# Kernel tuning notes

Hardware: AMD Instinct MI355X
Metric: run time of the kernel (lower is better)

## Reference

```python
import jax, jax.numpy as jnp
import numpy as np

N, E, B, H, L = 50000, 500000, 64, 64, 4


def setup_inputs() -> dict:
    key = jax.random.key(0)
    ks = jax.random.split(key, 32)
    def w(k, shp, fan_in):
        s = 1.0 / np.sqrt(fan_in)
        return jax.random.uniform(k, shp, jnp.float32, -s, s)
    inp = {
        "v0": jax.random.normal(ks[0], (N, 1), jnp.float32),
        "v1": jax.random.normal(ks[1], (N, 1), jnp.float32),
        "dist": jax.random.uniform(ks[2], (E, 1), jnp.float32),
        "edge_index": jax.random.randint(ks[3], (2, E), 0, N, jnp.int32),
        "batch": jnp.sort(jax.random.randint(ks[4], (N,), 0, B, jnp.int32)),
        "batch_size": B,
        # embeddings / per-input linears
        "wte": jax.random.normal(ks[5], (2, H), jnp.float32),
        "W_in0": w(ks[6], (H, 1), 1), "b_in0": w(ks[7], (H,), 1),
        "W_in1": w(ks[8], (H, 1), 1), "b_in1": w(ks[9], (H,), 1),
        "W_out0": w(ks[10], (1, H), H), "b_out0": w(ks[11], (1,), H),
        "W_out1": w(ks[12], (1, H), H), "b_out1": w(ks[13], (1,), H),
        "W_edge": w(ks[14], (H, 1), 1), "b_edge": w(ks[15], (H,), 1),
        # shared GraphBlock (ModuleList([block]*L) shares weights)
        "W_el": w(ks[16], (H, 2 * H), 2 * H), "b_el": w(ks[17], (H,), 2 * H),
        "W_n1": w(ks[18], (4 * H, 3 * H), 3 * H), "b_n1": w(ks[19], (4 * H,), 3 * H),
        "W_n2": w(ks[20], (H, 4 * H), 4 * H), "b_n2": w(ks[21], (H,), 4 * H),
        "W_gl": w(ks[22], (H, 2 * H), 2 * H), "b_gl": w(ks[23], (H,), 2 * H),
        # shared LSTMCell
        "W_ih": w(ks[24], (4 * H, H), H), "W_hh": w(ks[25], (4 * H, H), H),
        "b_ih": w(ks[26], (4 * H,), H), "b_hh": w(ks[27], (4 * H,), H),
    }
    return inp


def _forward(v0, v1, dist, edge_index, batch, batch_size,
             wte, W_in0, b_in0, W_in1, b_in1, W_out0, b_out0, W_out1, b_out1,
             W_edge, b_edge, W_el, b_el, W_n1, b_n1, W_n2, b_n2, W_gl, b_gl,
             W_ih, W_hh, b_ih, b_hh):
    # x = sum_i (type_embedding_i + Linear_i(v_i))  -> [N, H]
    x = (wte[0] + v0 @ W_in0.T + b_in0) + (wte[1] + v1 @ W_in1.T + b_in1)
    e = dist @ W_edge.T + b_edge                      # [E, H]
    u = jnp.zeros((batch_size, x.shape[-1]), x.dtype)  # [B, H]
    row, col = edge_index[0], edge_index[1]
    n_nodes = x.shape[0]
    cs = []
    for _ in range(L):  # shared weights across layers (faithful to [block]*L)
        # edge MLP on gathered source features, scatter-max to destination nodes
        msg = jax.nn.relu(jnp.concatenate([x[row], e], axis=-1) @ W_el.T + b_el)
        agg = jax.ops.segment_max(msg, col, num_segments=n_nodes)
        agg = jnp.where(jnp.isfinite(agg), agg, 0.0)  # empty segments -> 0
        # node MLP with residual
        h1 = jax.nn.relu(jnp.concatenate([agg, x, u[batch]], axis=-1) @ W_n1.T + b_n1)
        x = x + h1 @ W_n2.T + b_n2
        # global update: per-graph max over nodes
        x_u = jax.ops.segment_max(x, batch, num_segments=batch_size)
        x_u = jnp.where(jnp.isfinite(x_u), x_u, 0.0)
        u = u + jax.nn.relu(jnp.concatenate([x_u, u], axis=-1) @ W_gl.T + b_gl)
        # LSTMCell with zero initial (h, c) every layer (hidden_states=None path)
        gates = u @ W_ih.T + b_ih + b_hh  # h_prev = 0 so W_hh term vanishes
        i_g, f_g, g_g, o_g = jnp.split(gates, 4, axis=-1)
        c = jax.nn.sigmoid(i_g) * jnp.tanh(g_g)        # c_prev = 0
        u = jax.nn.sigmoid(o_g) * jnp.tanh(c)
        cs.append(c)
    outs = jnp.stack([x @ W_out0.T + b_out0, x @ W_out1.T + b_out1])  # [2, N, 1]
    return outs, jnp.stack(cs)  # ([2,N,1], [L,B,H])


def reference(v0, v1, dist, edge_index, batch, batch_size,
              wte, W_in0, b_in0, W_in1, b_in1, W_out0, b_out0, W_out1, b_out1,
              W_edge, b_edge, W_el, b_el, W_n1, b_n1, W_n2, b_n2, W_gl, b_gl,
              W_ih, W_hh, b_ih, b_hh):
    return _forward(v0, v1, dist, edge_index, batch, batch_size,
                    wte, W_in0, b_in0, W_in1, b_in1, W_out0, b_out0, W_out1, b_out1,
                    W_edge, b_edge, W_el, b_el, W_n1, b_n1, W_n2, b_n2, W_gl, b_gl,
                    W_ih, W_hh, b_ih, b_hh)
```

## Files before the change

kernel.cpp:

```cpp
#include <hip/hip_runtime.h>


typedef __attribute__((ext_vector_type(8))) short short8;
typedef __attribute__((ext_vector_type(4))) float f32x4;

__device__ __forceinline__ unsigned short f2bf(float f) {
  union { float f; unsigned u; } v; v.f = f;
  unsigned r = v.u + 0x7FFFu + ((v.u >> 16) & 1u);
  return (unsigned short)(r >> 16);
}
__device__ __forceinline__ float bf2f(unsigned short s) {
  return __uint_as_float((unsigned)s << 16);
}
__device__ __forceinline__ unsigned enc_ordered(float f) {
  unsigned u = __float_as_uint(f);
  return (u >> 31) ? ~u : (u | 0x80000000u);
}

__global__ void k_init(const float* __restrict__ v0, const float* __restrict__ v1,
                       const float* __restrict__ wte,
                       const float* __restrict__ Wi0, const float* __restrict__ bi0,
                       const float* __restrict__ Wi1, const float* __restrict__ bi1,
                       const int* __restrict__ batch,
                       int* __restrict__ gstart, int* __restrict__ gend,
                       float* __restrict__ x,
                       float* __restrict__ u, unsigned* __restrict__ xu_enc,
                       unsigned short* __restrict__ W1b, unsigned short* __restrict__ W2b,
                       unsigned short* __restrict__ Welb,
                       const float* __restrict__ W_n1, const float* __restrict__ W_n2,
                       const float* __restrict__ W_el,
                       const float* __restrict__ b_el,
                       const float* __restrict__ W_edge, const float* __restrict__ b_edge,
                       float* __restrict__ p, float* __restrict__ q,
                       float* __restrict__ c0, float* __restrict__ c1,
                       float* __restrict__ c2,
                       int* __restrict__ deg, int* __restrict__ cur, int N) {
  int gt = blockIdx.x * 256 + threadIdx.x;
  int NH = N * 64;
  if (gt < NH) {
    int n = gt >> 6, h = gt & 63;
    x[gt] = wte[h] + wte[64 + h] + bi0[h] + bi1[h] + v0[n] * Wi0[h] + v1[n] * Wi1[h];
    if (h == 0) {
      int bg = batch[n];
      if (n == 0 || batch[n - 1] != bg) gstart[bg] = n;
      if (n == N - 1 || batch[n + 1] != bg) gend[bg] = n + 1;
    }
    return;
  }
  int i = gt - NH;
  if (i < 4096) {
    u[i] = 0.f;
  } else if (i < 8192) {
    xu_enc[i - 4096] = 0x007FFFFFu;
  } else if (i < 8192 + 49152) {
    int j = i - 8192;
    W1b[j] = f2bf(W_n1[j]);
  } else if (i < 8192 + 49152 + 16384) {
    int j = i - 57344;
    W2b[j] = f2bf(W_n2[j]);
  } else if (i < 77824) {
    int j = i - 73728;
    Welb[j] = f2bf(W_el[(j >> 6) * 128 + (j & 63)]);
  } else if (i < 77824 + N) {
    deg[i - 77824] = 0;
  } else if (i < 77824 + 2 * N) {
    cur[i - 77824 - N] = 0;
  } else if (i < 77824 + 2 * N + 64) {
    int h = i - 77824 - 2 * N;
    float pp = 0.f, qq = 0.f, s0 = 0.f, s1 = 0.f, s2 = 0.f;
    for (int k = 0; k < 64; ++k) {
      float w2 = W_el[h * 128 + 64 + k];
      pp += w2 * W_edge[k];
      qq += w2 * b_edge[k];
      float w1 = W_el[h * 128 + k];
      float base = wte[k] + wte[64 + k] + bi0[k] + bi1[k];
      s0 += w1 * base;
      s1 += w1 * Wi0[k];
      s2 += w1 * Wi1[k];
    }
    p[h] = pp; q[h] = qq + b_el[h];
    c0[h] = s0; c1[h] = s1; c2[h] = s2;
  }
}

__global__ __launch_bounds__(256) void k_hist(const int* __restrict__ eidx,
                                              int* __restrict__ deg, int E) {
  int e = blockIdx.x * 256 + threadIdx.x;
  if (e < E) atomicAdd(&deg[eidx[E + e]], 1);
}

__global__ __launch_bounds__(256) void k_scan1(const int* __restrict__ deg,
                                               int* __restrict__ off,
                                               int* __restrict__ bsum, int N) {
  __shared__ int s[256];
  int b = blockIdx.x, t = threadIdx.x;
  int i0 = b * 512 + t * 2;
  int v0 = (i0 < N) ? deg[i0] : 0;
  int v1 = (i0 + 1 < N) ? deg[i0 + 1] : 0;
  int sum = v0 + v1;
  s[t] = sum;
  __syncthreads();
  for (int d = 1; d < 256; d <<= 1) {
    int val = (t >= d) ? s[t - d] : 0;
    __syncthreads();
    s[t] += val;
    __syncthreads();
  }
  int excl = s[t] - sum;
  if (i0 < N) off[i0] = excl + v0;
  if (i0 + 1 < N) off[i0 + 1] = excl + v0 + v1;
  if (t == 255) bsum[b] = s[t];
}

__global__ void k_scan2(int* __restrict__ bsum, int nb) {
  __shared__ int s[128];
  int t = threadIdx.x;
  int v = (t < nb) ? bsum[t] : 0;
  s[t] = v;
  __syncthreads();
  for (int d = 1; d < 128; d <<= 1) {
    int val = (t >= d) ? s[t - d] : 0;
    __syncthreads();
    s[t] += val;
    __syncthreads();
  }
  if (t < nb) bsum[t] = s[t] - v;
}

__global__ __launch_bounds__(256) void k_scatter(const int* __restrict__ eidx,
                                                 const float* __restrict__ dist,
                                                 const int* __restrict__ off,
                                                 const int* __restrict__ bsum,
                                                 int* __restrict__ cur,
                                                 uint2* __restrict__ spack, int E) {
  int e = blockIdx.x * 256 + threadIdx.x;
  if (e >= E) return;
  int c = eidx[E + e];
  int base = (c == 0) ? 0 : (off[c - 1] + bsum[(c - 1) >> 9]);
  int pos = base + atomicAdd(&cur[c], 1);
  spack[pos] = make_uint2((unsigned)eidx[e] | ((unsigned)(c & 31) << 27),
                          __float_as_uint(dist[e]));
}

template <int MODE>
__global__ __launch_bounds__(256) void k_node(
    const int* __restrict__ off, const int* __restrict__ bsum,
    const uint2* __restrict__ spack,
    const float* __restrict__ p, const float* __restrict__ q,
    const float* __restrict__ c0, const float* __restrict__ c1,
    const float* __restrict__ c2,
    const float* __restrict__ v0, const float* __restrict__ v1,
    float* __restrict__ x, unsigned short* __restrict__ y_bf,
    const int* __restrict__ batch, const float* __restrict__ u,
    const unsigned short* __restrict__ W1b, const unsigned short* __restrict__ W2b,
    const unsigned short* __restrict__ Welb,
    const float* __restrict__ b_n1, const float* __restrict__ b_n2,
    unsigned* __restrict__ xu_enc,
    float* __restrict__ bmaxA, float* __restrict__ bmaxB,
    int* __restrict__ bgidA, int* __restrict__ bgidB,
    const float* __restrict__ Wo0, const float* __restrict__ bo0,
    const float* __restrict__ Wo1, const float* __restrict__ bo1,
    float* __restrict__ outp, int N) {
  __shared__ __align__(16) char inb[32 * 384];
  __shared__ __align__(16) char h1T[32 * 512];
  __shared__ uint2 smeta[256];
  __shared__ int sgb[32];
  int t = threadIdx.x;
  int n0 = blockIdx.x * 32;
  int lane = t & 63, wv = t >> 6;
  int lr = lane & 15;
  int lk8 = (lane >> 4) << 3;
  int jo = (lane >> 4) << 2;
  int swzr = (lr & 7) << 4;
  int h0 = wv * 16 + jo;

  float4 xo[2];
#pragma unroll
  for (int nt = 0; nt < 2; ++nt) {
    int node = n0 + nt * 16 + lr;
    xo[nt] = (node < N) ? *(const float4*)(x + (size_t)node * 64 + h0)
                        : make_float4(0.f, 0.f, 0.f, 0.f);
  }
  int nd_s = t >> 3, ko = t & 7;
  int node_s = n0 + nd_s;
  float4 ua = make_float4(0.f, 0.f, 0.f, 0.f), ub = ua;
  if (node_s < N) {
    int g = batch[node_s];
    const float4* u4 = (const float4*)u;
    ua = u4[g * 16 + ko * 2];
    ub = u4[g * 16 + ko * 2 + 1];
  }
  if (t < 32) sgb[t] = batch[min(n0 + t, N - 1)];

  int* aggi = (int*)h1T;
#pragma unroll
  for (int i = 0; i < 8; ++i) aggi[t + i * 256] = 0;

#pragma unroll
  for (int nt = 0; nt < 2; ++nt) {
    int nd = nt * 16 + lr;
    unsigned lo = (unsigned)f2bf(xo[nt].x) | ((unsigned)f2bf(xo[nt].y) << 16);
    unsigned hi = (unsigned)f2bf(xo[nt].z) | ((unsigned)f2bf(xo[nt].w) << 16);
    *(uint2*)(inb + nd * 384 + ((128 + h0 * 2) ^ ((nd & 7) << 4))) = make_uint2(lo, hi);
  }
  {
    int swz = (nd_s & 7) << 4;
    uint4 uv;
    uv.x = f2bf(ua.x) | ((unsigned)f2bf(ua.y) << 16);
    uv.y = f2bf(ua.z) | ((unsigned)f2bf(ua.w) << 16);
    uv.z = f2bf(ub.x) | ((unsigned)f2bf(ub.y) << 16);
    uv.w = f2bf(ub.z) | ((unsigned)f2bf(ub.w) << 16);
    *(uint4*)(inb + nd_s * 384 + ((256 + ko * 16) ^ swz)) = uv;
  }
  __syncthreads();

  {
    int last = min(n0 + 31, N - 1);
    int ebase = (n0 == 0) ? 0 : (off[n0 - 1] + bsum[(n0 - 1) >> 9]);
    int eend = off[last] + bsum[last >> 9];
    int total = eend - ebase;
    int q4 = total >> 2;
    int wb = ebase + wv * q4;
    int we = (wv == 3) ? eend : (wb + q4);
    uint2* sm = smeta + wv * 64;
    int half = lane >> 5, l31 = lane & 31;
    const unsigned* y32 = (const unsigned*)y_bf + l31;
    float2 p2 = *(const float2*)(p + 2 * l31);
    float2 q2 = *(const float2*)(q + 2 * l31);
    float2 c02 = make_float2(0.f, 0.f), c12 = c02, c22 = c02;
    if (MODE == 0) {
      c02 = *(const float2*)(c0 + 2 * l31);
      c12 = *(const float2*)(c1 + 2 * l31);
      c22 = *(const float2*)(c2 + 2 * l31);
    }
    float m0 = 0.f, m1 = 0.f;
    int ccur = -1;
    uint2 r = make_uint2(0u, 0u);
    if (wb < we) {
      int cnt = min(64, we - wb);
      if (lane < cnt) r = spack[wb + lane];
    }
    for (int cb = wb; cb < we; cb += 64) {
      int ccnt = min(64, we - cb);
      sm[lane] = r;
      int nb = cb + 64;
      if (nb < we) {
        int ncnt = we - nb;
        if (lane < ncnt) r = spack[nb + lane];
      }
      int nfull = ccnt >> 1;
      int i = 0;
      for (; i + 8 <= nfull; i += 8) {
        uint2 e[8]; unsigned yd[8]; float va[8], vb[8];
#pragma unroll
        for (int k = 0; k < 8; ++k) e[k] = sm[2 * (i + k) + half];
#pragma unroll
        for (int k = 0; k < 8; ++k) {
          unsigned row = e[k].x & 0x07FFFFFFu;
          if (MODE == 0) { va[k] = v0[row]; vb[k] = v1[row]; }
          else yd[k] = y32[row << 5];
        }
#pragma unroll
        for (int k = 0; k < 8; ++k) {
          float y0f, y1f;
          if (MODE == 0) {
            y0f = fmaf(vb[k], c22.x, fmaf(va[k], c12.x, c02.x));
            y1f = fmaf(vb[k], c22.y, fmaf(va[k], c12.y, c02.y));
          } else {
            y0f = __uint_as_float(yd[k] << 16);
            y1f = __uint_as_float(yd[k] & 0xFFFF0000u);
          }
          float d = __uint_as_float(e[k].y);
          float g0 = fmaxf(fmaf(d, p2.x, y0f + q2.x), 0.f);
          float g1 = fmaxf(fmaf(d, p2.y, y1f + q2.y), 0.f);
          int c = (int)(e[k].x >> 27);
          if (c != ccur) {
            if (ccur >= 0) {
              atomicMax(&aggi[ccur * 64 + 2 * l31], __float_as_int(m0));
              atomicMax(&aggi[ccur * 64 + 2 * l31 + 1], __float_as_int(m1));
            }
            ccur = c; m0 = g0; m1 = g1;
          } else { m0 = fmaxf(m0, g0); m1 = fmaxf(m1, g1); }
        }
      }
      for (; 2 * i < ccnt; ++i) {
        int idx = 2 * i + half;
        bool val = idx < ccnt;
        uint2 e = sm[val ? idx : 0];
        unsigned row = e.x & 0x07FFFFFFu;
        float y0f, y1f;
        if (MODE == 0) {
          float a = v0[row], b = v1[row];
          y0f = fmaf(b, c22.x, fmaf(a, c12.x, c02.x));
          y1f = fmaf(b, c22.y, fmaf(a, c12.y, c02.y));
        } else {
          unsigned yd = y32[row << 5];
          y0f = __uint_as_float(yd << 16);
          y1f = __uint_as_float(yd & 0xFFFF0000u);
        }
        float d = __uint_as_float(e.y);
        float g0 = val ? fmaxf(fmaf(d, p2.x, y0f + q2.x), 0.f) : 0.f;
        float g1 = val ? fmaxf(fmaf(d, p2.y, y1f + q2.y), 0.f) : 0.f;
        int c = val ? (int)(e.x >> 27) : ccur;
        if (c != ccur) {
          if (ccur >= 0) {
            atomicMax(&aggi[ccur * 64 + 2 * l31], __float_as_int(m0));
            atomicMax(&aggi[ccur * 64 + 2 * l31 + 1], __float_as_int(m1));
          }
          ccur = c; m0 = g0; m1 = g1;
        } else { m0 = fmaxf(m0, g0); m1 = fmaxf(m1, g1); }
      }
    }
    if (ccur >= 0) {
      atomicMax(&aggi[ccur * 64 + 2 * l31], __float_as_int(m0));
      atomicMax(&aggi[ccur * 64 + 2 * l31 + 1], __float_as_int(m1));
    }
  }
  __syncthreads();

  {
    int swz = (nd_s & 7) << 4;
    const float4* ag4 = (const float4*)(h1T);
    float4 aa = ag4[nd_s * 16 + ko * 2];
    float4 ab = ag4[nd_s * 16 + ko * 2 + 1];
    uint4 av;
    av.x = f2bf(aa.x) | ((unsigned)f2bf(aa.y) << 16);
    av.y = f2bf(aa.z) | ((unsigned)f2bf(aa.w) << 16);
    av.z = f2bf(ab.x) | ((unsigned)f2bf(ab.y) << 16);
    av.w = f2bf(ab.z) | ((unsigned)f2bf(ab.w) << 16);
    *(uint4*)(inb + nd_s * 384 + ((ko * 16) ^ swz)) = av;
  }
  __syncthreads();

  int w = wv;

  f32x4 acc[4][2];
#pragma unroll
  for (int ot = 0; ot < 4; ++ot)
#pragma unroll
    for (int nt = 0; nt < 2; ++nt) acc[ot][nt] = (f32x4){0.f, 0.f, 0.f, 0.f};
  const unsigned short* W1p = W1b + (w * 64 + lr) * 192 + lk8;
#pragma unroll
  for (int ks = 0; ks < 6; ++ks) {
    int kb = ks * 64 + lk8 * 2;
    short8 b0 = *(const short8*)(inb + lr * 384 + (kb ^ swzr));
    short8 b1 = *(const short8*)(inb + (16 + lr) * 384 + (kb ^ swzr));
#pragma unroll
    for (int ot = 0; ot < 4; ++ot) {
      short8 a = *(const short8*)(W1p + ot * (16 * 192) + ks * 32);
      acc[ot][0] = __builtin_amdgcn_mfma_f32_16x16x32_bf16(a, b0, acc[ot][0], 0, 0, 0);
      acc[ot][1] = __builtin_amdgcn_mfma_f32_16x16x32_bf16(a, b1, acc[ot][1], 0, 0, 0);
    }
  }
  __syncthreads();
#pragma unroll
  for (int ot = 0; ot < 4; ++ot) {
    int o = w * 64 + ot * 16 + jo;
    float4 bs = *(const float4*)(b_n1 + o);
#pragma unroll
    for (int nt = 0; nt < 2; ++nt) {
      int nd = nt * 16 + lr;
      unsigned lo = (unsigned)f2bf(fmaxf(acc[ot][nt][0] + bs.x, 0.f)) |
                    ((unsigned)f2bf(fmaxf(acc[ot][nt][1] + bs.y, 0.f)) << 16);
      unsigned hi = (unsigned)f2bf(fmaxf(acc[ot][nt][2] + bs.z, 0.f)) |
                    ((unsigned)f2bf(fmaxf(acc[ot][nt][3] + bs.w, 0.f)) << 16);
      *(uint2*)(h1T + nd * 512 + ((o * 2) ^ ((nd & 7) << 4))) = make_uint2(lo, hi);
    }
  }
  __syncthreads();

  f32x4 acc2[2] = {{0.f, 0.f, 0.f, 0.f}, {0.f, 0.f, 0.f, 0.f}};
  const unsigned short* W2p = W2b + (w * 16 + lr) * 256 + lk8;
#pragma unroll
  for (int ks = 0; ks < 8; ++ks) {
    short8 a = *(const short8*)(W2p + ks * 32);
    int kb = ks * 64 + lk8 * 2;
    short8 b0 = *(const short8*)(h1T + lr * 512 + (kb ^ swzr));
    short8 b1 = *(const short8*)(h1T + (16 + lr) * 512 + (kb ^ swzr));
    acc2[0] = __builtin_amdgcn_mfma_f32_16x16x32_bf16(a, b0, acc2[0], 0, 0, 0);
    acc2[1] = __builtin_amdgcn_mfma_f32_16x16x32_bf16(a, b1, acc2[1], 0, 0, 0);
  }
  float4 b2 = *(const float4*)(b_n2 + h0);
  char* xnb = inb;
  float4 xn[2];
#pragma unroll
  for (int nt = 0; nt < 2; ++nt) {
    int nd = nt * 16 + lr;
    int node = n0 + nd;
    xn[nt].x = xo[nt].x + acc2[nt][0] + b2.x;
    xn[nt].y = xo[nt].y + acc2[nt][1] + b2.y;
    xn[nt].z = xo[nt].z + acc2[nt][2] + b2.z;
    xn[nt].w = xo[nt].w + acc2[nt][3] + b2.w;
    if (node >= N) xn[nt] = make_float4(0.f, 0.f, 0.f, 0.f);
    if (MODE != 2 && node < N) *(float4*)(x + (size_t)node * 64 + h0) = xn[nt];
    if (MODE != 2) {
      unsigned lo = (unsigned)f2bf(xn[nt].x) | ((unsigned)f2bf(xn[nt].y) << 16);
      unsigned hi = (unsigned)f2bf(xn[nt].z) | ((unsigned)f2bf(xn[nt].w) << 16);
      *(uint2*)(xnb + nd * 128 + ((h0 * 2) ^ ((nd & 7) << 4))) = make_uint2(lo, hi);
    }
  }

  {
    const float NEG = -__builtin_huge_valf();
    int gA = sgb[0], gB = sgb[31];
    float a0 = NEG, a1 = NEG, a2 = NEG, a3 = NEG;
    float e0 = NEG, e1 = NEG, e2 = NEG, e3 = NEG;
#pragma unroll
    for (int nt = 0; nt < 2; ++nt) {
      int nd = nt * 16 + lr;
      if (n0 + nd < N) {
        int g = sgb[nd];
        if (g == gA) {
          a0 = fmaxf(a0, xn[nt].x); a1 = fmaxf(a1, xn[nt].y);
          a2 = fmaxf(a2, xn[nt].z); a3 = fmaxf(a3, xn[nt].w);
        } else if (g == gB) {
          e0 = fmaxf(e0, xn[nt].x); e1 = fmaxf(e1, xn[nt].y);
          e2 = fmaxf(e2, xn[nt].z); e3 = fmaxf(e3, xn[nt].w);
        } else {
          unsigned* xe = xu_enc + g * 64 + h0;
          atomicMax(xe + 0, enc_ordered(xn[nt].x));
          atomicMax(xe + 1, enc_ordered(xn[nt].y));
          atomicMax(xe + 2, enc_ordered(xn[nt].z));
          atomicMax(xe + 3, enc_ordered(xn[nt].w));
        }
      }
    }
#pragma unroll
    for (int msk = 1; msk <= 8; msk <<= 1) {
      a0 = fmaxf(a0, __shfl_xor(a0, msk)); a1 = fmaxf(a1, __shfl_xor(a1, msk));
      a2 = fmaxf(a2, __shfl_xor(a2, msk)); a3 = fmaxf(a3, __shfl_xor(a3, msk));
      e0 = fmaxf(e0, __shfl_xor(e0, msk)); e1 = fmaxf(e1, __shfl_xor(e1, msk));
      e2 = fmaxf(e2, __shfl_xor(e2, msk)); e3 = fmaxf(e3, __shfl_xor(e3, msk));
    }
    if (lr == 0) {
      size_t base = (size_t)blockIdx.x * 64 + h0;
      bmaxA[base + 0] = a0; bmaxA[base + 1] = a1;
      bmaxA[base + 2] = a2; bmaxA[base + 3] = a3;
      bmaxB[base + 0] = e0; bmaxB[base + 1] = e1;
      bmaxB[base + 2] = e2; bmaxB[base + 3] = e3;
    }
    if (t == 0) {
      bgidA[blockIdx.x] = gA;
      bgidB[blockIdx.x] = (gB == gA) ? -1 : gB;
    }
  }
  __syncthreads();

  if (MODE != 2) {
    f32x4 acc3[2] = {{0.f, 0.f, 0.f, 0.f}, {0.f, 0.f, 0.f, 0.f}};
    const unsigned short* W3p = Welb + (w * 16 + lr) * 64 + lk8;
#pragma unroll
    for (int ks = 0; ks < 2; ++ks) {
      short8 a = *(const short8*)(W3p + ks * 32);
      int kb = ks * 64 + lk8 * 2;
      short8 b0 = *(const short8*)(xnb + lr * 128 + (kb ^ swzr));
      short8 b1 = *(const short8*)(xnb + (16 + lr) * 128 + (kb ^ swzr));
      acc3[0] = __builtin_amdgcn_mfma_f32_16x16x32_bf16(a, b0, acc3[0], 0, 0, 0);
      acc3[1] = __builtin_amdgcn_mfma_f32_16x16x32_bf16(a, b1, acc3[1], 0, 0, 0);
    }
    int o0 = w * 16 + jo;
#pragma unroll
    for (int nt = 0; nt < 2; ++nt) {
      int node = n0 + nt * 16 + lr;
      if (node < N) {
        unsigned lo = (unsigned)f2bf(acc3[nt][0]) | ((unsigned)f2bf(acc3[nt][1]) << 16);
        unsigned hi = (unsigned)f2bf(acc3[nt][2]) | ((unsigned)f2bf(acc3[nt][3]) << 16);
        *(uint2*)(y_bf + (size_t)node * 64 + o0) = make_uint2(lo, hi);
      }
    }
  } else {
    float4 w0 = *(const float4*)(Wo0 + h0);
    float4 w1 = *(const float4*)(Wo1 + h0);
    float* ow = (float*)h1T;
#pragma unroll
    for (int nt = 0; nt < 2; ++nt) {
      float p0 = xn[nt].x * w0.x + xn[nt].y * w0.y + xn[nt].z * w0.z + xn[nt].w * w0.w;
      float p1 = xn[nt].x * w1.x + xn[nt].y * w1.y + xn[nt].z * w1.z + xn[nt].w * w1.w;
      p0 += __shfl_xor(p0, 16); p0 += __shfl_xor(p0, 32);
      p1 += __shfl_xor(p1, 16); p1 += __shfl_xor(p1, 32);
      if (lane < 16) {
        ow[w * 64 + 0 + nt * 16 + lr] = p0;
        ow[w * 64 + 32 + nt * 16 + lr] = p1;
      }
    }
    __syncthreads();
    if (t < 64) {
      int oi = t >> 5, nd = t & 31;
      int node = n0 + nd;
      if (node < N) {
        float v = ow[0 * 64 + oi * 32 + nd] + ow[1 * 64 + oi * 32 + nd] +
                  ow[2 * 64 + oi * 32 + nd] + ow[3 * 64 + oi * 32 + nd];
        v += (oi ? bo1[0] : bo0[0]);
        outp[(size_t)oi * N + node] = v;
      }
    }
  }
}

__global__ __launch_bounds__(256) void k_graph(const int* __restrict__ gstart,
                                               const int* __restrict__ gend,
                                               const float* __restrict__ bmaxA,
                                               const float* __restrict__ bmaxB,
                                               const int* __restrict__ bgidA,
                                               const int* __restrict__ bgidB,
                                               unsigned* __restrict__ xu_enc,
                                               float* __restrict__ u,
                                               const float* __restrict__ W_gl,
                                               const float* __restrict__ b_gl,
                                               const float* __restrict__ W_ih,
                                               const float* __restrict__ b_ih,
                                               const float* __restrict__ b_hh,
                                               float* __restrict__ c_out) {
  __shared__ float red[4][3][64];
  __shared__ float xu_s[64], us[64], un[64];
  int g = blockIdx.x;
  int t = threadIdx.x, h = t & 63, qd = t >> 6;
  const float NEG = -__builtin_huge_valf();

  float m = NEG;
  int gs = gstart[g], ge = gend[g];
  if (gs < ge) {
    int bs = gs >> 5, be = (ge - 1) >> 5;
    for (int b = bs + qd; b <= be; b += 4) {
      if (bgidA[b] == g) m = fmaxf(m, bmaxA[(size_t)b * 64 + h]);
      if (bgidB[b] == g) m = fmaxf(m, bmaxB[(size_t)b * 64 + h]);
    }
  }
  red[qd][0][h] = m;
  __syncthreads();
  if (qd == 0) {
    m = fmaxf(fmaxf(red[0][0][h], red[1][0][h]), fmaxf(red[2][0][h], red[3][0][h]));
    unsigned Ev = xu_enc[g * 64 + h];
    float fd = (Ev & 0x80000000u) ? __uint_as_float(Ev & 0x7FFFFFFFu)
                                  : __uint_as_float(~Ev);
    m = fmaxf(m, fd);
    xu_enc[g * 64 + h] = 0x007FFFFFu;
    xu_s[h] = isfinite(m) ? m : 0.f;
    us[h] = u[g * 64 + h];
  }
  __syncthreads();

  float pre = 0.f;
  {
    const float* Wrow = W_gl + h * 128 + qd * 32;
    const float* src = (qd < 2) ? (xu_s + qd * 32) : (us + (qd - 2) * 32);
#pragma unroll 8
    for (int k = 0; k < 32; ++k) pre += src[k] * Wrow[k];
  }
  red[qd][0][h] = pre;
  __syncthreads();
  if (qd == 0) {
    float prs = red[0][0][h] + red[1][0][h] + red[2][0][h] + red[3][0][h] + b_gl[h];
    un[h] = us[h] + fmaxf(prs, 0.f);
  }
  __syncthreads();

  float gi = 0.f, gg = 0.f, go = 0.f;
#pragma unroll 4
  for (int k = qd * 16; k < qd * 16 + 16; ++k) {
    float uv = un[k];
    gi += uv * W_ih[h * 64 + k];
    gg += uv * W_ih[(128 + h) * 64 + k];
    go += uv * W_ih[(192 + h) * 64 + k];
  }
  red[qd][0][h] = gi; red[qd][1][h] = gg; red[qd][2][h] = go;
  __syncthreads();
  if (qd == 0) {
    gi = red[0][0][h] + red[1][0][h] + red[2][0][h] + red[3][0][h] + b_ih[h] + b_hh[h];
    gg = red[0][1][h] + red[1][1][h] + red[2][1][h] + red[3][1][h] +
         b_ih[128 + h] + b_hh[128 + h];
    go = red[0][2][h] + red[1][2][h] + red[2][2][h] + red[3][2][h] +
         b_ih[192 + h] + b_hh[192 + h];
    float cc = (1.f / (1.f + expf(-gi))) * tanhf(gg);
    float u2v = (1.f / (1.f + expf(-go))) * tanhf(cc);
    c_out[g * 64 + h] = cc;
    u[g * 64 + h] = u2v;
  }
}

extern "C" void kernel_launch(void* const* d_in, const int* in_sizes, int n_in,
                              void* d_out, int out_size, void* d_ws, size_t ws_size,
                              hipStream_t stream) {
  const float* v0 = (const float*)d_in[0];
  const float* v1 = (const float*)d_in[1];
  const float* dist = (const float*)d_in[2];
  const int* eidx = (const int*)d_in[3];
  const int* batch = (const int*)d_in[4];
  const float* wte = (const float*)d_in[6];
  const float* Wi0 = (const float*)d_in[7];
  const float* bi0 = (const float*)d_in[8];
  const float* Wi1 = (const float*)d_in[9];
  const float* bi1 = (const float*)d_in[10];
  const float* Wo0 = (const float*)d_in[11];
  const float* bo0 = (const float*)d_in[12];
  const float* Wo1 = (const float*)d_in[13];
  const float* bo1 = (const float*)d_in[14];
  const float* W_edge = (const float*)d_in[15];
  const float* b_edge = (const float*)d_in[16];
  const float* W_el = (const float*)d_in[17];
  const float* b_el = (const float*)d_in[18];
  const float* W_n1 = (const float*)d_in[19];
  const float* b_n1 = (const float*)d_in[20];
  const float* W_n2 = (const float*)d_in[21];
  const float* b_n2 = (const float*)d_in[22];
  const float* W_gl = (const float*)d_in[23];
  const float* b_gl = (const float*)d_in[24];
  const float* W_ih = (const float*)d_in[25];
  const float* b_ih = (const float*)d_in[27];
  const float* b_hh = (const float*)d_in[28];

  const int N = in_sizes[0];
  const int E = in_sizes[2];
  const int NH = N * 64;
  const int NB512 = (N + 511) / 512;
  const int nblk = (N + 31) / 32;

  float* ws = (float*)d_ws;
  float* x = ws;
  float* u = x + NH;
  unsigned* xu_enc = (unsigned*)(u + 4096);
  float* p = (float*)(xu_enc + 4096);
  float* q = p + 64;
  float* c0 = q + 64;
  float* c1 = c0 + 64;
  float* c2 = c1 + 64;
  unsigned short* W1b = (unsigned short*)(c2 + 64);
  unsigned short* W2b = W1b + 49152;
  unsigned short* Welb = W2b + 16384;
  unsigned short* y_bf = Welb + 4096;
  int* deg = (int*)(y_bf + NH);
  int* off = deg + N;
  int* cur = off + N;
  int* bsum = cur + N;
  int* gstart = bsum + 128;
  int* gend = gstart + 64;
  int* bgidA = gend + 64;
  int* bgidB = bgidA + nblk;
  float* bmaxA = (float*)(bgidB + nblk);
  float* bmaxB = bmaxA + (size_t)nblk * 64;
  uint2* spack = (uint2*)(((size_t)(bmaxB + (size_t)nblk * 64) + 15) & ~(size_t)15);

  float* outp = (float*)d_out;

  k_init<<<(NH + 77824 + 2 * N + 64 + 255) / 256, 256, 0, stream>>>(
      v0, v1, wte, Wi0, bi0, Wi1, bi1, batch, gstart, gend, x,
      u, xu_enc, W1b, W2b, Welb, W_n1, W_n2, W_el, b_el, W_edge, b_edge,
      p, q, c0, c1, c2, deg, cur, N);
  k_hist<<<(E + 255) / 256, 256, 0, stream>>>(eidx, deg, E);
  k_scan1<<<NB512, 256, 0, stream>>>(deg, off, bsum, N);
  k_scan2<<<1, 128, 0, stream>>>(bsum, NB512);
  k_scatter<<<(E + 255) / 256, 256, 0, stream>>>(eidx, dist, off, bsum, cur, spack, E);

  for (int l = 0; l < 4; ++l) {
    if (l == 0) {
      k_node<0><<<nblk, 256, 0, stream>>>(off, bsum, spack, p, q, c0, c1, c2, v0, v1,
                                          x, y_bf, batch, u, W1b, W2b, Welb, b_n1, b_n2,
                                          xu_enc, bmaxA, bmaxB, bgidA, bgidB,
                                          Wo0, bo0, Wo1, bo1, outp, N);
    } else if (l < 3) {
      k_node<1><<<nblk, 256, 0, stream>>>(off, bsum, spack, p, q, c0, c1, c2, v0, v1,
                                          x, y_bf, batch, u, W1b, W2b, Welb, b_n1, b_n2,
                                          xu_enc, bmaxA, bmaxB, bgidA, bgidB,
                                          Wo0, bo0, Wo1, bo1, outp, N);
    } else {
      k_node<2><<<nblk, 256, 0, stream>>>(off, bsum, spack, p, q, c0, c1, c2, v0, v1,
                                          x, y_bf, batch, u, W1b, W2b, Welb, b_n1, b_n2,
                                          xu_enc, bmaxA, bmaxB, bgidA, bgidB,
                                          Wo0, bo0, Wo1, bo1, outp, N);
    }
    k_graph<<<64, 256, 0, stream>>>(gstart, gend, bmaxA, bmaxB, bgidA, bgidB,
                                    xu_enc, u, W_gl, b_gl, W_ih, b_ih, b_hh,
                                    outp + 2 * N + l * 4096);
  }
}
```

Before: 313.9 us.

## Compute initial node features in first layer kernel and halve MLP hidden LDS

The initial node embedding x is no longer written to global memory by the init kernel. The layer-0 node kernel now computes it on the fly from v0/v1 and the small weight vectors, which removes a write and a read of the N×64 float array. The node MLP is also split into two halves of the 256-wide hidden layer, so the bf16 hidden buffer in LDS shrinks from 16KB to 8KB. That should allow more resident blocks, at the cost of an extra barrier and a second pass over the first matmul's input tiles.

```diff
diff --git a/kernel.cpp b/kernel.cpp
--- a/kernel.cpp
+++ b/kernel.cpp
@@ -23,7 +23,6 @@
                        const float* __restrict__ Wi1, const float* __restrict__ bi1,
                        const int* __restrict__ batch,
                        int* __restrict__ gstart, int* __restrict__ gend,
-                       float* __restrict__ x,
                        float* __restrict__ u, unsigned* __restrict__ xu_enc,
                        unsigned short* __restrict__ W1b, unsigned short* __restrict__ W2b,
                        unsigned short* __restrict__ Welb,
@@ -35,19 +34,7 @@
                        float* __restrict__ c0, float* __restrict__ c1,
                        float* __restrict__ c2,
                        int* __restrict__ deg, int* __restrict__ cur, int N) {
-  int gt = blockIdx.x * 256 + threadIdx.x;
-  int NH = N * 64;
-  if (gt < NH) {
-    int n = gt >> 6, h = gt & 63;
-    x[gt] = wte[h] + wte[64 + h] + bi0[h] + bi1[h] + v0[n] * Wi0[h] + v1[n] * Wi1[h];
-    if (h == 0) {
-      int bg = batch[n];
-      if (n == 0 || batch[n - 1] != bg) gstart[bg] = n;
-      if (n == N - 1 || batch[n + 1] != bg) gend[bg] = n + 1;
-    }
-    return;
-  }
-  int i = gt - NH;
+  int i = blockIdx.x * 256 + threadIdx.x;
   if (i < 4096) {
     u[i] = 0.f;
   } else if (i < 8192) {
@@ -65,8 +52,13 @@
     deg[i - 77824] = 0;
   } else if (i < 77824 + 2 * N) {
     cur[i - 77824 - N] = 0;
-  } else if (i < 77824 + 2 * N + 64) {
-    int h = i - 77824 - 2 * N;
+  } else if (i < 77824 + 3 * N) {
+    int n = i - 77824 - 2 * N;
+    int bg = batch[n];
+    if (n == 0 || batch[n - 1] != bg) gstart[bg] = n;
+    if (n == N - 1 || batch[n + 1] != bg) gend[bg] = n + 1;
+  } else if (i < 77824 + 3 * N + 64) {
+    int h = i - 77824 - 3 * N;
     float pp = 0.f, qq = 0.f, s0 = 0.f, s1 = 0.f, s2 = 0.f;
     for (int k = 0; k < 64; ++k) {
       float w2 = W_el[h * 128 + 64 + k];
@@ -150,6 +142,9 @@
     const float* __restrict__ c0, const float* __restrict__ c1,
     const float* __restrict__ c2,
     const float* __restrict__ v0, const float* __restrict__ v1,
+    const float* __restrict__ wte,
+    const float* __restrict__ Wi0, const float* __restrict__ bi0,
+    const float* __restrict__ Wi1, const float* __restrict__ bi1,
     float* __restrict__ x, unsigned short* __restrict__ y_bf,
     const int* __restrict__ batch, const float* __restrict__ u,
     const unsigned short* __restrict__ W1b, const unsigned short* __restrict__ W2b,
@@ -162,7 +157,7 @@
     const float* __restrict__ Wo1, const float* __restrict__ bo1,
     float* __restrict__ outp, int N) {
   __shared__ __align__(16) char inb[32 * 384];
-  __shared__ __align__(16) char h1T[32 * 512];
+  __shared__ __align__(16) char h1h[32 * 256];
   __shared__ uint2 smeta[256];
   __shared__ int sgb[32];
   int t = threadIdx.x;
@@ -175,11 +170,32 @@
   int h0 = wv * 16 + jo;
 
   float4 xo[2];
-#pragma unroll
-  for (int nt = 0; nt < 2; ++nt) {
-    int node = n0 + nt * 16 + lr;
-    xo[nt] = (node < N) ? *(const float4*)(x + (size_t)node * 64 + h0)
-                        : make_float4(0.f, 0.f, 0.f, 0.f);
+  if (MODE == 0) {
+    float4 wA = *(const float4*)(wte + h0);
+    float4 wB = *(const float4*)(wte + 64 + h0);
+    float4 bA = *(const float4*)(bi0 + h0);
+    float4 bB = *(const float4*)(bi1 + h0);
+    float4 w0v = *(const float4*)(Wi0 + h0);
+    float4 w1v = *(const float4*)(Wi1 + h0);
+    float4 cb = make_float4(wA.x + wB.x + bA.x + bB.x, wA.y + wB.y + bA.y + bB.y,
+                            wA.z + wB.z + bA.z + bB.z, wA.w + wB.w + bA.w + bB.w);
+#pragma unroll
+    for (int nt = 0; nt < 2; ++nt) {
+      int node = n0 + nt * 16 + lr;
+      float a = (node < N) ? v0[node] : 0.f;
+      float b = (node < N) ? v1[node] : 0.f;
+      xo[nt].x = cb.x + a * w0v.x + b * w1v.x;
+      xo[nt].y = cb.y + a * w0v.y + b * w1v.y;
+      xo[nt].z = cb.z + a * w0v.z + b * w1v.z;
+      xo[nt].w = cb.w + a * w0v.w + b * w1v.w;
+    }
+  } else {
+#pragma unroll
+    for (int nt = 0; nt < 2; ++nt) {
+      int node = n0 + nt * 16 + lr;
+      xo[nt] = (node < N) ? *(const float4*)(x + (size_t)node * 64 + h0)
+                          : make_float4(0.f, 0.f, 0.f, 0.f);
+    }
   }
   int nd_s = t >> 3, ko = t & 7;
   int node_s = n0 + nd_s;
@@ -192,7 +208,7 @@
   }
   if (t < 32) sgb[t] = batch[min(n0 + t, N - 1)];
 
-  int* aggi = (int*)h1T;
+  int* aggi = (int*)h1h;
 #pragma unroll
   for (int i = 0; i < 8; ++i) aggi[t + i * 256] = 0;
 
@@ -320,7 +336,7 @@
 
   {
     int swz = (nd_s & 7) << 4;
-    const float4* ag4 = (const float4*)(h1T);
+    const float4* ag4 = (const float4*)(h1h);
     float4 aa = ag4[nd_s * 16 + ko * 2];
     float4 ab = ag4[nd_s * 16 + ko * 2 + 1];
     uint4 av;
@@ -334,52 +350,56 @@
 
   int w = wv;
 
-  f32x4 acc[4][2];
-#pragma unroll
-  for (int ot = 0; ot < 4; ++ot)
-#pragma unroll
-    for (int nt = 0; nt < 2; ++nt) acc[ot][nt] = (f32x4){0.f, 0.f, 0.f, 0.f};
-  const unsigned short* W1p = W1b + (w * 64 + lr) * 192 + lk8;
-#pragma unroll
-  for (int ks = 0; ks < 6; ++ks) {
-    int kb = ks * 64 + lk8 * 2;
-    short8 b0 = *(const short8*)(inb + lr * 384 + (kb ^ swzr));
-    short8 b1 = *(const short8*)(inb + (16 + lr) * 384 + (kb ^ swzr));
-#pragma unroll
-    for (int ot = 0; ot < 4; ++ot) {
-      short8 a = *(const short8*)(W1p + ot * (16 * 192) + ks * 32);
-      acc[ot][0] = __builtin_amdgcn_mfma_f32_16x16x32_bf16(a, b0, acc[ot][0], 0, 0, 0);
-      acc[ot][1] = __builtin_amdgcn_mfma_f32_16x16x32_bf16(a, b1, acc[ot][1], 0, 0, 0);
-    }
-  }
-  __syncthreads();
-#pragma unroll
-  for (int ot = 0; ot < 4; ++ot) {
-    int o = w * 64 + ot * 16 + jo;
-    float4 bs = *(const float4*)(b_n1 + o);
-#pragma unroll
-    for (int nt = 0; nt < 2; ++nt) {
-      int nd = nt * 16 + lr;
-      unsigned lo = (unsigned)f2bf(fmaxf(acc[ot][nt][0] + bs.x, 0.f)) |
-                    ((unsigned)f2bf(fmaxf(acc[ot][nt][1] + bs.y, 0.f)) << 16);
-      unsigned hi = (unsigned)f2bf(fmaxf(acc[ot][nt][2] + bs.z, 0.f)) |
-                    ((unsigned)f2bf(fmaxf(acc[ot][nt][3] + bs.w, 0.f)) << 16);
-      *(uint2*)(h1T + nd * 512 + ((o * 2) ^ ((nd & 7) << 4))) = make_uint2(lo, hi);
-    }
-  }
-  __syncthreads();
-
   f32x4 acc2[2] = {{0.f, 0.f, 0.f, 0.f}, {0.f, 0.f, 0.f, 0.f}};
-  const unsigned short* W2p = W2b + (w * 16 + lr) * 256 + lk8;
-#pragma unroll
-  for (int ks = 0; ks < 8; ++ks) {
-    short8 a = *(const short8*)(W2p + ks * 32);
-    int kb = ks * 64 + lk8 * 2;
-    short8 b0 = *(const short8*)(h1T + lr * 512 + (kb ^ swzr));
-    short8 b1 = *(const short8*)(h1T + (16 + lr) * 512 + (kb ^ swzr));
-    acc2[0] = __builtin_amdgcn_mfma_f32_16x16x32_bf16(a, b0, acc2[0], 0, 0, 0);
-    acc2[1] = __builtin_amdgcn_mfma_f32_16x16x32_bf16(a, b1, acc2[1], 0, 0, 0);
-  }
+#pragma unroll
+  for (int H = 0; H < 2; ++H) {
+    f32x4 acc[2][2];
+#pragma unroll
+    for (int ot = 0; ot < 2; ++ot)
+#pragma unroll
+      for (int nt = 0; nt < 2; ++nt) acc[ot][nt] = (f32x4){0.f, 0.f, 0.f, 0.f};
+    const unsigned short* W1p = W1b + (size_t)(H * 128 + w * 32 + lr) * 192 + lk8;
+#pragma unroll
+    for (int ks = 0; ks < 6; ++ks) {
+      int kb = ks * 64 + lk8 * 2;
+      short8 b0 = *(const short8*)(inb + lr * 384 + (kb ^ swzr));
+      short8 b1 = *(const short8*)(inb + (16 + lr) * 384 + (kb ^ swzr));
+#pragma unroll
+      for (int ot = 0; ot < 2; ++ot) {
+        short8 a = *(const short8*)(W1p + ot * (16 * 192) + ks * 32);
+        acc[ot][0] = __builtin_amdgcn_mfma_f32_16x16x32_bf16(a, b0, acc[ot][0], 0, 0, 0);
+        acc[ot][1] = __builtin_amdgcn_mfma_f32_16x16x32_bf16(a, b1, acc[ot][1], 0, 0, 0);
+      }
+    }
+#pragma unroll
+    for (int ot = 0; ot < 2; ++ot) {
+      int o = H * 128 + w * 32 + ot * 16 + jo;
+      float4 bs = *(const float4*)(b_n1 + o);
+      int ol = (w * 32 + ot * 16 + jo) * 2;
+#pragma unroll
+      for (int nt = 0; nt < 2; ++nt) {
+        int nd = nt * 16 + lr;
+        unsigned lo = (unsigned)f2bf(fmaxf(acc[ot][nt][0] + bs.x, 0.f)) |
+                      ((unsigned)f2bf(fmaxf(acc[ot][nt][1] + bs.y, 0.f)) << 16);
+        unsigned hi = (unsigned)f2bf(fmaxf(acc[ot][nt][2] + bs.z, 0.f)) |
+                      ((unsigned)f2bf(fmaxf(acc[ot][nt][3] + bs.w, 0.f)) << 16);
+        *(uint2*)(h1h + nd * 256 + (ol ^ ((nd & 7) << 4))) = make_uint2(lo, hi);
+      }
+    }
+    __syncthreads();
+    const unsigned short* W2p = W2b + (w * 16 + lr) * 256 + H * 128 + lk8;
+#pragma unroll
+    for (int ks = 0; ks < 4; ++ks) {
+      short8 a = *(const short8*)(W2p + ks * 32);
+      int kb = ks * 64 + lk8 * 2;
+      short8 b0 = *(const short8*)(h1h + lr * 256 + (kb ^ swzr));
+      short8 b1 = *(const short8*)(h1h + (16 + lr) * 256 + (kb ^ swzr));
+      acc2[0] = __builtin_amdgcn_mfma_f32_16x16x32_bf16(a, b0, acc2[0], 0, 0, 0);
+      acc2[1] = __builtin_amdgcn_mfma_f32_16x16x32_bf16(a, b1, acc2[1], 0, 0, 0);
+    }
+    if (H == 0) __syncthreads();
+  }
+
   float4 b2 = *(const float4*)(b_n2 + h0);
   char* xnb = inb;
   float4 xn[2];
@@ -471,7 +491,7 @@
   } else {
     float4 w0 = *(const float4*)(Wo0 + h0);
     float4 w1 = *(const float4*)(Wo1 + h0);
-    float* ow = (float*)h1T;
+    float* ow = (float*)h1h;
 #pragma unroll
     for (int nt = 0; nt < 2; ++nt) {
       float p0 = xn[nt].x * w0.x + xn[nt].y * w0.y + xn[nt].z * w0.z + xn[nt].w * w0.w;
@@ -642,8 +662,8 @@
 
   float* outp = (float*)d_out;
 
-  k_init<<<(NH + 77824 + 2 * N + 64 + 255) / 256, 256, 0, stream>>>(
-      v0, v1, wte, Wi0, bi0, Wi1, bi1, batch, gstart, gend, x,
+  k_init<<<(77824 + 3 * N + 64 + 255) / 256, 256, 0, stream>>>(
+      v0, v1, wte, Wi0, bi0, Wi1, bi1, batch, gstart, gend,
       u, xu_enc, W1b, W2b, Welb, W_n1, W_n2, W_el, b_el, W_edge, b_edge,
       p, q, c0, c1, c2, deg, cur, N);
   k_hist<<<(E + 255) / 256, 256, 0, stream>>>(eidx, deg, E);
@@ -654,16 +674,19 @@
   for (int l = 0; l < 4; ++l) {
     if (l == 0) {
       k_node<0><<<nblk, 256, 0, stream>>>(off, bsum, spack, p, q, c0, c1, c2, v0, v1,
+                                          wte, Wi0, bi0, Wi1, bi1,
                                           x, y_bf, batch, u, W1b, W2b, Welb, b_n1, b_n2,
                                           xu_enc, bmaxA, bmaxB, bgidA, bgidB,
                                           Wo0, bo0, Wo1, bo1, outp, N);
     } else if (l < 3) {
       k_node<1><<<nblk, 256, 0, stream>>>(off, bsum, spack, p, q, c0, c1, c2, v0, v1,
+                                          wte, Wi0, bi0, Wi1, bi1,
                                           x, y_bf, batch, u, W1b, W2b, Welb, b_n1, b_n2,
                                           xu_enc, bmaxA, bmaxB, bgidA, bgidB,
                                           Wo0, bo0, Wo1, bo1, outp, N);
     } else {
       k_node<2><<<nblk, 256, 0, stream>>>(off, bsum, spack, p, q, c0, c1, c2, v0, v1,
+                                          wte, Wi0, bi0, Wi1, bi1,
                                           x, y_bf, batch, u, W1b, W2b, Welb, b_n1, b_n2,
                                           xu_enc, bmaxA, bmaxB, bgidA, bgidB,
                                           Wo0, bo0, Wo1, bo1, outp, N);
```

Result: no change. 309.8 us, median of 2 (-1.3%).
